# Performance work log

Measured on AMD Instinct MI355X. Metric: run time of the kernel, lower is better.

The kernel has to match this reference:

```python
import jax, jax.numpy as jnp
import numpy as np

B, S, H, UNITS = 32, 2048, 1024, 1024


def setup_inputs() -> dict:
    key = jax.random.key(0)
    ks = jax.random.split(key, 5)
    scale = 1.0 / np.sqrt(H)
    return {
        "query": jax.random.normal(ks[0], (B, H), dtype=jnp.float32),
        "values": jax.random.normal(ks[1], (B, S, H), dtype=jnp.float32),
        "W1": jax.random.normal(ks[2], (H, UNITS), dtype=jnp.float32) * scale,
        "b1": jnp.zeros((UNITS,), dtype=jnp.float32),
        "W2": jax.random.normal(ks[3], (H, UNITS), dtype=jnp.float32) * scale,
        "b2": jnp.zeros((UNITS,), dtype=jnp.float32),
        "V": jax.random.normal(ks[4], (UNITS, 1), dtype=jnp.float32) * (1.0 / np.sqrt(UNITS)),
        "bV": jnp.zeros((1,), dtype=jnp.float32),
    }


def reference(query, values, W1, b1, W2, b2, V, bV):
    # W1(values): [B,S,U]; W2(query): [B,1,U] broadcast over S
    proj_v = jnp.einsum("bsh,hu->bsu", values, W1) + b1
    proj_q = (query @ W2 + b2)[:, None, :]
    score = jnp.tanh(proj_v + proj_q) @ V + bV          # [B,S,1]
    attention_weights = jax.nn.softmax(score, axis=1)   # softmax over seq
    context_vector = jnp.sum(attention_weights * values, axis=1)  # [B,H]
    return (attention_weights, context_vector)
```

## Files before the change

### kernel.cpp

```cpp
#include <hip/hip_runtime.h>
#include <hip/hip_bf16.h>
#include <stdint.h>

#define B_ 32
#define S_ 2048
#define H_ 1024
#define U_ 1024

typedef __attribute__((ext_vector_type(8))) short short8;
typedef __attribute__((ext_vector_type(4))) float f32x4;

#define AS1 __attribute__((address_space(1)))
#define AS3 __attribute__((address_space(3)))
#define FENCE __builtin_amdgcn_sched_barrier(0)

__device__ __forceinline__ unsigned short f2bf(float f) {
  unsigned int u = __float_as_uint(f);
  u += 0x7fffu + ((u >> 16) & 1u);
  return (unsigned short)(u >> 16);
}

__global__ void k_transpose_w1(const float* __restrict__ W1, unsigned short* __restrict__ W1T) {
  __shared__ float tile[64][65];
  const int tx = threadIdx.x, ty = threadIdx.y;
  const int u0 = blockIdx.x * 64, h0 = blockIdx.y * 64;
#pragma unroll
  for (int i = 0; i < 16; ++i) {
    int hl = ty + i * 4;
    tile[hl][tx] = W1[(size_t)(h0 + hl) * U_ + (u0 + tx)];
  }
  __syncthreads();
#pragma unroll
  for (int i = 0; i < 16; ++i) {
    int ul = ty + i * 4;
    W1T[(size_t)(u0 + ul) * H_ + (h0 + tx)] = f2bf(tile[tx][ul]);
  }
}

__global__ void k_b1q_part(const float* __restrict__ query, const float* __restrict__ W2,
                           float* __restrict__ qpart) {
  __shared__ float q_sh[32 * 128];
  const int u = blockIdx.x * 256 + threadIdx.x;
  const int hs = blockIdx.y;
  for (int i = threadIdx.x; i < 4096; i += 256) {
    const int b = i >> 7, h = i & 127;
    q_sh[i] = query[b * H_ + hs * 128 + h];
  }
  __syncthreads();
  float acc[32];
#pragma unroll
  for (int b = 0; b < 32; ++b) acc[b] = 0.f;
  for (int h = 0; h < 128; ++h) {
    const float w = W2[(size_t)(hs * 128 + h) * U_ + u];
#pragma unroll
    for (int b = 0; b < 32; ++b) acc[b] += q_sh[b * 128 + h] * w;
  }
#pragma unroll
  for (int b = 0; b < 32; ++b) qpart[((size_t)hs * 32 + b) * U_ + u] = acc[b];
}

__global__ void k_b1q_comb(const float* __restrict__ qpart, const float* __restrict__ b1,
                           const float* __restrict__ b2, float* __restrict__ b1q) {
  const int u = blockIdx.x * 256 + threadIdx.x;
  const int b = blockIdx.y;
  float s = b1[u] + b2[u];
#pragma unroll
  for (int hs = 0; hs < 8; ++hs) s += qpart[((size_t)hs * 32 + b) * U_ + u];
  b1q[b * U_ + u] = s;
}

#define BM 128
#define BN 256
#define BK 32
#define NSTEP 32

__global__ __launch_bounds__(512, 4)
void k_fused_score(const float* __restrict__ values,
                   const unsigned short* __restrict__ W1T,
                   const float* __restrict__ b1q, const float* __restrict__ V,
                   float* __restrict__ score_part) {
  __shared__ __align__(16) unsigned char smem[65536];
  unsigned short* As = (unsigned short*)smem;
  unsigned short* Bs = (unsigned short*)(smem + 16384);
  float* scorebuf = (float*)smem;

  const int tid = threadIdx.x;
  const int g = blockIdx.x;
  const int seq = (g & 7) * 256 + (g >> 3);
  const int bn = seq & 3;
  const int bm = seq >> 2;

  const int lane = tid & 63, wid = tid >> 6;
  const int wm = wid >> 2, wn = wid & 3;
  const int u0 = bn * BN;

  const int arow = tid >> 2;
  const int alc  = tid & 3;
  const int aplc = alc ^ ((arow >> 1) & 3);
  const float* aSrcF = values + (size_t)(bm * BM + arow) * H_ + alc * 8;
  const int awoff = arow * 32 + aplc * 8;

  const unsigned short* bSrc0 = W1T + (size_t)(u0 + arow) * H_ + aplc * 8;
  const unsigned short* bSrc1 = bSrc0 + (size_t)128 * H_;

  const int l15 = lane & 15, l16 = lane >> 4;
  const int fsq = ((l16 ^ ((lane >> 1) & 3)) << 3);
  const int pA = (wm * 64 + l15) * 32 + fsq;
  const int pB = (wn * 64 + l15) * 32 + fsq;

  f32x4 acc[4][4];
#pragma unroll
  for (int mf = 0; mf < 4; ++mf)
#pragma unroll
    for (int nf = 0; nf < 4; ++nf) acc[mf][nf] = (f32x4){0.f, 0.f, 0.f, 0.f};

  float4 aX0, aX1, aY0, aY1;

#define ISSUE_SET(P0, P1, tt) { \
    const float4* p_ = (const float4*)(aSrcF + (tt) * BK); \
    P0 = p_[0]; P1 = p_[1]; }

#define WRITE_SET(P0, P1, slot) { \
    short8 w_; \
    w_[0]=f2bf(P0.x); w_[1]=f2bf(P0.y); w_[2]=f2bf(P0.z); w_[3]=f2bf(P0.w); \
    w_[4]=f2bf(P1.x); w_[5]=f2bf(P1.y); w_[6]=f2bf(P1.z); w_[7]=f2bf(P1.w); \
    *(short8*)&As[(slot) * 4096 + awoff] = w_; }

#define STAGE_B(tt, slot) { \
    const int ko_ = (tt) * BK; \
    __builtin_amdgcn_global_load_lds((const AS1 void*)(bSrc0 + ko_), \
        (AS3 void*)&Bs[(slot) * 8192 + tid * 8], 16, 0, 0); \
    __builtin_amdgcn_global_load_lds((const AS1 void*)(bSrc1 + ko_), \
        (AS3 void*)&Bs[(slot) * 8192 + 4096 + tid * 8], 16, 0, 0); }

#define SUBSTEP(T, ASLOT, RI0, RI1, RW0, RW1) { \
    if ((T) + 2 < NSTEP) { \
      ISSUE_SET(RI0, RI1, (T) + 2); \
      STAGE_B((T) + 2, ((T) + 2) % 3); \
    } \
    FENCE; \
    short8 af[4], bv[4]; \
    const int bO_ = ((T) % 3) * 8192; \
    _Pragma("unroll") \
    for (int mf = 0; mf < 4; ++mf) \
      af[mf] = *(const short8*)&As[(ASLOT) * 4096 + pA + mf * 512]; \
    _Pragma("unroll") \
    for (int nf = 0; nf < 4; ++nf) \
      bv[nf] = *(const short8*)&Bs[bO_ + pB + nf * 512]; \
    _Pragma("unroll") \
    for (int nf = 0; nf < 4; ++nf) \
      _Pragma("unroll") \
      for (int mf = 0; mf < 4; ++mf) \
        acc[mf][nf] = __builtin_amdgcn_mfma_f32_16x16x32_bf16(af[mf], bv[nf], acc[mf][nf], 0, 0, 0); \
    FENCE; \
    if ((T) + 2 < NSTEP) { asm volatile("s_waitcnt vmcnt(4)" ::: "memory"); } \
    else                 { asm volatile("s_waitcnt vmcnt(0)" ::: "memory"); } \
    if ((T) + 1 < NSTEP) { WRITE_SET(RW0, RW1, ((T) + 1) & 1); } \
    asm volatile("s_waitcnt lgkmcnt(0)" ::: "memory"); \
    FENCE; \
    __builtin_amdgcn_s_barrier(); }

  ISSUE_SET(aX0, aX1, 0);
  ISSUE_SET(aY0, aY1, 1);
  STAGE_B(0, 0);
  STAGE_B(1, 1);
  asm volatile("s_waitcnt vmcnt(6)" ::: "memory");
  WRITE_SET(aX0, aX1, 0);
  asm volatile("s_waitcnt vmcnt(2)" ::: "memory");
  asm volatile("s_waitcnt lgkmcnt(0)" ::: "memory");
  FENCE;
  __builtin_amdgcn_s_barrier();

  for (int t = 0; t < NSTEP; t += 2) {
    SUBSTEP(t,     0, aX0, aX1, aY0, aY1);
    SUBSTEP(t + 1, 1, aY0, aY1, aX0, aX1);
  }

  __syncthreads();
  const int b_blk = bm >> 4;
  float bqv[4], vvv[4];
#pragma unroll
  for (int nf = 0; nf < 4; ++nf) {
    const int ug = u0 + wn * 64 + nf * 16 + l15;
    bqv[nf] = b1q[b_blk * U_ + ug];
    vvv[nf] = V[ug];
  }
  float rp[4][4];
#pragma unroll
  for (int mf = 0; mf < 4; ++mf)
#pragma unroll
    for (int j = 0; j < 4; ++j) rp[mf][j] = 0.f;
#pragma unroll
  for (int nf = 0; nf < 4; ++nf)
#pragma unroll
    for (int mf = 0; mf < 4; ++mf) {
      const f32x4 c = acc[mf][nf];
#pragma unroll
      for (int j = 0; j < 4; ++j) {
        const float x = c[j] + bqv[nf];
        const float e = __expf(2.f * x);
        const float tt = 1.f - 2.f / (e + 1.f);
        rp[mf][j] += tt * vvv[nf];
      }
    }
#pragma unroll
  for (int mf = 0; mf < 4; ++mf)
#pragma unroll
    for (int j = 0; j < 4; ++j) {
      float v = rp[mf][j];
      v += __shfl_xor(v, 1);
      v += __shfl_xor(v, 2);
      v += __shfl_xor(v, 4);
      v += __shfl_xor(v, 8);
      rp[mf][j] = v;
    }
  if (l15 == 0) {
#pragma unroll
    for (int mf = 0; mf < 4; ++mf)
#pragma unroll
      for (int j = 0; j < 4; ++j)
        scorebuf[(wm * 64 + mf * 16 + l16 * 4 + j) * 4 + wn] = rp[mf][j];
  }
  __syncthreads();
  if (tid < BM) {
    const float s = scorebuf[tid * 4 + 0] + scorebuf[tid * 4 + 1] +
                    scorebuf[tid * 4 + 2] + scorebuf[tid * 4 + 3];
    score_part[(size_t)bn * (B_ * S_) + bm * BM + tid] = s;
  }
}

__global__ void k_softmax(const float* __restrict__ sp, float* __restrict__ aw) {
  __shared__ float red[8];
  const int b = blockIdx.x, tid = threadIdx.x;
  const int BS = B_ * S_;
  float x[8];
  float m = -1e30f;
#pragma unroll
  for (int i = 0; i < 8; ++i) {
    const int s = b * S_ + tid + i * 256;
    x[i] = sp[s] + sp[BS + s] + sp[2 * BS + s] + sp[3 * BS + s];
    m = fmaxf(m, x[i]);
  }
#pragma unroll
  for (int off = 32; off; off >>= 1) m = fmaxf(m, __shfl_xor(m, off));
  if ((tid & 63) == 0) red[tid >> 6] = m;
  __syncthreads();
  m = fmaxf(fmaxf(red[0], red[1]), fmaxf(red[2], red[3]));
  float e[8];
  float sum = 0.f;
#pragma unroll
  for (int i = 0; i < 8; ++i) { e[i] = __expf(x[i] - m); sum += e[i]; }
#pragma unroll
  for (int off = 32; off; off >>= 1) sum += __shfl_xor(sum, off);
  __syncthreads();
  if ((tid & 63) == 0) red[4 + (tid >> 6)] = sum;
  __syncthreads();
  sum = red[4] + red[5] + red[6] + red[7];
  const float inv = 1.f / sum;
#pragma unroll
  for (int i = 0; i < 8; ++i) aw[b * S_ + tid + i * 256] = e[i] * inv;
}

__global__ void k_ctx_partial(const float* __restrict__ values, const float* __restrict__ aw,
                              float* __restrict__ part) {
  __shared__ float a_s[64];
  const int b = blockIdx.y, sc = blockIdx.x, tid = threadIdx.x;
  if (tid < 64) a_s[tid] = aw[b * S_ + sc * 64 + tid];
  __syncthreads();
  const float4* vp = (const float4*)values + (size_t)(b * S_ + sc * 64) * (H_ / 4) + tid;
  float4 acc = {0.f, 0.f, 0.f, 0.f};
#pragma unroll 4
  for (int i = 0; i < 64; ++i) {
    const float4 v = vp[(size_t)i * (H_ / 4)];
    const float a = a_s[i];
    acc.x += a * v.x; acc.y += a * v.y; acc.z += a * v.z; acc.w += a * v.w;
  }
  ((float4*)part)[(size_t)(b * 32 + sc) * (H_ / 4) + tid] = acc;
}

__global__ void k_ctx_combine(const float* __restrict__ part, float* __restrict__ ctx) {
  const int b = blockIdx.x, tid = threadIdx.x;
  float4 s = {0.f, 0.f, 0.f, 0.f};
#pragma unroll
  for (int c = 0; c < 32; ++c) {
    const float4 v = ((const float4*)part)[(size_t)(b * 32 + c) * (H_ / 4) + tid];
    s.x += v.x; s.y += v.y; s.z += v.z; s.w += v.w;
  }
  ((float4*)ctx)[b * (H_ / 4) + tid] = s;
}

extern "C" void kernel_launch(void* const* d_in, const int* in_sizes, int n_in,
                              void* d_out, int out_size, void* d_ws, size_t ws_size,
                              hipStream_t stream) {
  const float* query  = (const float*)d_in[0];
  const float* values = (const float*)d_in[1];
  const float* W1     = (const float*)d_in[2];
  const float* b1     = (const float*)d_in[3];
  const float* W2     = (const float*)d_in[4];
  const float* b2     = (const float*)d_in[5];
  const float* V      = (const float*)d_in[6];

  char* ws = (char*)d_ws;
  unsigned short* W1T = (unsigned short*)ws;
  float* b1q   = (float*)(ws + 2u * 1024u * 1024u);
  float* spart = (float*)(ws + 2u * 1024u * 1024u + 128u * 1024u);
  float* qpart = (float*)(ws + 3u * 1024u * 1024u + 128u * 1024u);
  float* cpart = (float*)(ws + 4u * 1024u * 1024u + 256u * 1024u);

  float* aw  = (float*)d_out;
  float* ctx = aw + B_ * S_;

  k_transpose_w1<<<dim3(16, 16), dim3(64, 4), 0, stream>>>(W1, W1T);
  k_b1q_part<<<dim3(4, 8), dim3(256), 0, stream>>>(query, W2, qpart);
  k_b1q_comb<<<dim3(4, 32), dim3(256), 0, stream>>>(qpart, b1, b2, b1q);
  k_fused_score<<<dim3(2048), dim3(512), 0, stream>>>(values, W1T, b1q, V, spart);
  k_softmax<<<dim3(32), dim3(256), 0, stream>>>(spart, aw);
  k_ctx_partial<<<dim3(32, 32), dim3(256), 0, stream>>>(values, aw, cpart);
  k_ctx_combine<<<dim3(32), dim3(256), 0, stream>>>(cpart, ctx);
}
```

Before: 283.5 us.

## Load W1T operand directly into registers instead of staging through LDS

The B operand (bf16 W1T) no longer goes through a triple-buffered LDS stage via global_load_lds. Each wave now double-buffers its own 64 rows of B in registers with plain global loads, one k-step ahead. This cuts shared memory from 64KB to 16KB and removes the LDS reads for B, which could let more blocks fit per CU. In exchange, the two M-waves that share the same B columns both fetch it, doubling B traffic into the cache hierarchy, and register pressure rises. Latency hiding is now only one step deep instead of two.

```diff
diff --git a/kernel.cpp b/kernel.cpp
--- a/kernel.cpp
+++ b/kernel.cpp
@@ -79,9 +79,8 @@
                    const unsigned short* __restrict__ W1T,
                    const float* __restrict__ b1q, const float* __restrict__ V,
                    float* __restrict__ score_part) {
-  __shared__ __align__(16) unsigned char smem[65536];
+  __shared__ __align__(16) unsigned char smem[16384];
   unsigned short* As = (unsigned short*)smem;
-  unsigned short* Bs = (unsigned short*)(smem + 16384);
   float* scorebuf = (float*)smem;
 
   const int tid = threadIdx.x;
@@ -100,13 +99,11 @@
   const float* aSrcF = values + (size_t)(bm * BM + arow) * H_ + alc * 8;
   const int awoff = arow * 32 + aplc * 8;
 
-  const unsigned short* bSrc0 = W1T + (size_t)(u0 + arow) * H_ + aplc * 8;
-  const unsigned short* bSrc1 = bSrc0 + (size_t)128 * H_;
-
   const int l15 = lane & 15, l16 = lane >> 4;
   const int fsq = ((l16 ^ ((lane >> 1) & 3)) << 3);
   const int pA = (wm * 64 + l15) * 32 + fsq;
-  const int pB = (wn * 64 + l15) * 32 + fsq;
+
+  const unsigned short* bSrcR = W1T + (size_t)(u0 + wn * 64 + l15) * H_ + l16 * 8;
 
   f32x4 acc[4][4];
 #pragma unroll
@@ -115,6 +112,7 @@
     for (int nf = 0; nf < 4; ++nf) acc[mf][nf] = (f32x4){0.f, 0.f, 0.f, 0.f};
 
   float4 aX0, aX1, aY0, aY1;
+  short8 bX[4], bY[4];
 
 #define ISSUE_SET(P0, P1, tt) { \
     const float4* p_ = (const float4*)(aSrcF + (tt) * BK); \
@@ -126,54 +124,46 @@
     w_[4]=f2bf(P1.x); w_[5]=f2bf(P1.y); w_[6]=f2bf(P1.z); w_[7]=f2bf(P1.w); \
     *(short8*)&As[(slot) * 4096 + awoff] = w_; }
 
-#define STAGE_B(tt, slot) { \
-    const int ko_ = (tt) * BK; \
-    __builtin_amdgcn_global_load_lds((const AS1 void*)(bSrc0 + ko_), \
-        (AS3 void*)&Bs[(slot) * 8192 + tid * 8], 16, 0, 0); \
-    __builtin_amdgcn_global_load_lds((const AS1 void*)(bSrc1 + ko_), \
-        (AS3 void*)&Bs[(slot) * 8192 + 4096 + tid * 8], 16, 0, 0); }
-
-#define SUBSTEP(T, ASLOT, RI0, RI1, RW0, RW1) { \
-    if ((T) + 2 < NSTEP) { \
-      ISSUE_SET(RI0, RI1, (T) + 2); \
-      STAGE_B((T) + 2, ((T) + 2) % 3); \
-    } \
+#define ISSUE_B(REG, tt) { \
+    _Pragma("unroll") \
+    for (int nf_ = 0; nf_ < 4; ++nf_) \
+      REG[nf_] = *(const short8*)(bSrcR + (size_t)nf_ * 16 * H_ + (tt) * BK); }
+
+#define SUBSTEP(T, ASLOT, RI0, RI1, RW0, RW1, BCUR, BNXT) { \
+    if ((T) + 2 < NSTEP) { ISSUE_SET(RI0, RI1, (T) + 2); } \
+    if ((T) + 1 < NSTEP) { ISSUE_B(BNXT, (T) + 1); } \
     FENCE; \
-    short8 af[4], bv[4]; \
-    const int bO_ = ((T) % 3) * 8192; \
+    short8 af[4]; \
     _Pragma("unroll") \
     for (int mf = 0; mf < 4; ++mf) \
       af[mf] = *(const short8*)&As[(ASLOT) * 4096 + pA + mf * 512]; \
     _Pragma("unroll") \
     for (int nf = 0; nf < 4; ++nf) \
-      bv[nf] = *(const short8*)&Bs[bO_ + pB + nf * 512]; \
-    _Pragma("unroll") \
-    for (int nf = 0; nf < 4; ++nf) \
       _Pragma("unroll") \
       for (int mf = 0; mf < 4; ++mf) \
-        acc[mf][nf] = __builtin_amdgcn_mfma_f32_16x16x32_bf16(af[mf], bv[nf], acc[mf][nf], 0, 0, 0); \
+        acc[mf][nf] = __builtin_amdgcn_mfma_f32_16x16x32_bf16(af[mf], BCUR[nf], acc[mf][nf], 0, 0, 0); \
     FENCE; \
-    if ((T) + 2 < NSTEP) { asm volatile("s_waitcnt vmcnt(4)" ::: "memory"); } \
-    else                 { asm volatile("s_waitcnt vmcnt(0)" ::: "memory"); } \
-    if ((T) + 1 < NSTEP) { WRITE_SET(RW0, RW1, ((T) + 1) & 1); } \
-    asm volatile("s_waitcnt lgkmcnt(0)" ::: "memory"); \
+    if ((T) + 2 < NSTEP)      { asm volatile("s_waitcnt vmcnt(6)" ::: "memory"); } \
+    else if ((T) + 1 < NSTEP) { asm volatile("s_waitcnt vmcnt(4)" ::: "memory"); } \
+    if ((T) + 1 < NSTEP) { \
+      WRITE_SET(RW0, RW1, ((T) + 1) & 1); \
+      asm volatile("s_waitcnt lgkmcnt(0)" ::: "memory"); \
+    } \
     FENCE; \
     __builtin_amdgcn_s_barrier(); }
 
   ISSUE_SET(aX0, aX1, 0);
   ISSUE_SET(aY0, aY1, 1);
-  STAGE_B(0, 0);
-  STAGE_B(1, 1);
+  ISSUE_B(bX, 0);
   asm volatile("s_waitcnt vmcnt(6)" ::: "memory");
   WRITE_SET(aX0, aX1, 0);
-  asm volatile("s_waitcnt vmcnt(2)" ::: "memory");
   asm volatile("s_waitcnt lgkmcnt(0)" ::: "memory");
   FENCE;
   __builtin_amdgcn_s_barrier();
 
   for (int t = 0; t < NSTEP; t += 2) {
-    SUBSTEP(t,     0, aX0, aX1, aY0, aY1);
-    SUBSTEP(t + 1, 1, aY0, aY1, aX0, aX1);
+    SUBSTEP(t,     0, aX0, aX1, aY0, aY1, bX, bY);
+    SUBSTEP(t + 1, 1, aY0, aY1, aX0, aX1, bY, bX);
   }
 
   __syncthreads();
```

Measured after the change: 631.4 us. 123% more time.
